# Kernel tuning notes

Hardware: AMD Instinct MI355X
Metric: run time of the kernel (lower is better)

## Reference

```python
import jax, jax.numpy as jnp
import numpy as np

B, L, H, D = 64, 2048, 1024, 128  # segments, segment length, hidden, input_dim
N = B * L

def swish(z):
    return z * jax.nn.sigmoid(z)

def setup_inputs() -> dict:
    key = jax.random.key(0)
    ks = jax.random.split(key, 10)
    s = 0.02
    x_seeds = jax.random.normal(ks[0], (N, D), dtype=jnp.float32)
    x_nodes = jax.random.normal(ks[1], (N, D), dtype=jnp.float32)
    W_seed = jax.random.normal(ks[2], (H, D), dtype=jnp.float32) * s
    W_node = jax.random.normal(ks[3], (H, D), dtype=jnp.float32) * s
    W1 = jax.random.normal(ks[4], (H, H), dtype=jnp.float32) * s
    b1 = jnp.zeros((H,), dtype=jnp.float32)
    W2 = jax.random.normal(ks[5], (H, H), dtype=jnp.float32) * s
    b2 = jnp.zeros((H,), dtype=jnp.float32)
    w_ns = jax.random.normal(ks[6], (1, H), dtype=jnp.float32) * s   # node_score_layer (zero-init in src; random for nontrivial baseline)
    W_stop = jax.random.normal(ks[7], (2, H), dtype=jnp.float32) * s  # stopping_score_layer
    starts = jnp.arange(B, dtype=jnp.int32) * L
    indptr = jnp.stack([starts, starts + L, starts + L], axis=1)  # (start, end, candidate_end)
    return {"x_seeds": x_seeds, "x_nodes": x_nodes, "W_seed": W_seed, "W_node": W_node,
            "W1": W1, "b1": b1, "W2": W2, "b2": b2, "w_ns": w_ns, "W_stop": W_stop,
            "indptr": indptr}

def reference(x_seeds, x_nodes, W_seed, W_node, W1, b1, W2, b2, w_ns, W_stop, indptr):
    # embeddings + 2-layer Swish MLP
    h = x_seeds @ W_seed.T + x_nodes @ W_node.T            # [N, H]
    h = swish(h @ W1.T + b1)
    h = swish(h @ W2.T + b2)
    node_scores = (h @ w_ns.T)[:, 0]                       # [N]
    # ragged segments (uniform length L) defined by indptr starts
    nb = indptr.shape[0]
    seg_len = h.shape[0] // nb                             # static L
    idx = indptr[:, 0][:, None] + jnp.arange(seg_len)      # [B, L]
    h_seg = h[idx]                                         # [B, L, H]
    stop_node = h_seg.mean(axis=1)                         # [B, H] per-segment mean pool
    node_logits = jax.nn.log_softmax(node_scores[idx], axis=1)          # [B, L]
    stop_logits = jax.nn.log_softmax(stop_node @ W_stop.T, axis=1)      # [B, 2]
    # concat([node_logits + stop0, stop1]) per segment
    return jnp.concatenate([node_logits + stop_logits[:, :1], stop_logits[:, 1:]], axis=1)  # [B, L+1]
```

## Files before the change

### kernel.cpp

```cpp
#include <hip/hip_runtime.h>

typedef float f32x4 __attribute__((ext_vector_type(4)));
typedef __bf16 bf16x8 __attribute__((ext_vector_type(8)));
typedef unsigned short u16x8 __attribute__((ext_vector_type(8)));

#define DEVINL static __device__ __forceinline__

DEVINL unsigned short f2bf(float f) {
    unsigned int u = __builtin_bit_cast(unsigned int, f);
    u += 0x7fffu + ((u >> 16) & 1u);
    return (unsigned short)(u >> 16);
}
DEVINL float bf2f(unsigned short u) {
    unsigned int x = ((unsigned int)u) << 16;
    return __builtin_bit_cast(float, x);
}

#define GLD16(gp, lp)                                                          \
    __builtin_amdgcn_global_load_lds(                                          \
        (const __attribute__((address_space(1))) void*)(gp),                   \
        (__attribute__((address_space(3))) void*)(lp), 16, 0, 0)

__global__ void pack_cat_k(const float* __restrict__ s0, const float* __restrict__ s1,
                           unsigned short* __restrict__ dst, int nchunks) {
    int e = blockIdx.x * 256 + threadIdx.x;
    if (e >= nchunks) return;
    int row = e >> 5, ch = e & 31;
    const float* src = (ch < 16) ? (s0 + (size_t)row * 128 + ch * 8)
                                 : (s1 + (size_t)row * 128 + (ch - 16) * 8);
    float4 a = *(const float4*)src;
    float4 b = *(const float4*)(src + 4);
    u16x8 o;
    o[0] = f2bf(a.x); o[1] = f2bf(a.y); o[2] = f2bf(a.z); o[3] = f2bf(a.w);
    o[4] = f2bf(b.x); o[5] = f2bf(b.y); o[6] = f2bf(b.z); o[7] = f2bf(b.w);
    *(u16x8*)(dst + (size_t)e * 8) = o;
}

__global__ void cvt_k(const float* __restrict__ s, unsigned short* __restrict__ d, int nchunks) {
    int e = blockIdx.x * 256 + threadIdx.x;
    if (e >= nchunks) return;
    float4 a = *(const float4*)(s + (size_t)e * 8);
    float4 b = *(const float4*)(s + (size_t)e * 8 + 4);
    u16x8 o;
    o[0] = f2bf(a.x); o[1] = f2bf(a.y); o[2] = f2bf(a.z); o[3] = f2bf(a.w);
    o[4] = f2bf(b.x); o[5] = f2bf(b.y); o[6] = f2bf(b.z); o[7] = f2bf(b.w);
    *(u16x8*)(d + (size_t)e * 8) = o;
}

template <int EPI>
__global__ void gemm_bt_k(const unsigned short* __restrict__ A,
                          const unsigned short* __restrict__ B,
                          const float* __restrict__ bias,
                          unsigned short* __restrict__ C,
                          const float* __restrict__ wns,
                          float* __restrict__ sc,
                          float* __restrict__ pl,
                          int M, int N, int K) {
    __shared__ unsigned short As[128 * 32];
    __shared__ unsigned short Bs[128 * 32];
    const int tid  = threadIdx.x;
    const int lane = tid & 63;
    const int wv   = tid >> 6;
    const int wr   = wv >> 1, wc = wv & 1;
    const int ntn  = N >> 7;

    const int nwg = gridDim.x;
    const int xcd = blockIdx.x & 7, blk = blockIdx.x >> 3;
    const int q = nwg >> 3, rr = nwg & 7;
    const int logical = (xcd < rr ? xcd * (q + 1) : rr * (q + 1) + (xcd - rr) * q) + blk;

    const int im   = logical / ntn, in = logical % ntn;
    const size_t rowA0 = (size_t)im * 128, rowB0 = (size_t)in * 128;

    const int e0 = tid, e1 = tid + 256;
    const int ra0 = e0 >> 2, ca0 = (e0 & 3) * 8;
    const int ra1 = e1 >> 2, ca1 = (e1 & 3) * 8;

    f32x4 acc[4][4] = {};

    const int frow = lane & 15;
    const int kb   = (lane >> 4) * 8;

    for (int k0 = 0; k0 < K; k0 += 32) {
        GLD16(A + (rowA0 + ra0) * K + k0 + ca0, (char*)As + e0 * 16);
        GLD16(A + (rowA0 + ra1) * K + k0 + ca1, (char*)As + e1 * 16);
        GLD16(B + (rowB0 + ra0) * K + k0 + ca0, (char*)Bs + e0 * 16);
        GLD16(B + (rowB0 + ra1) * K + k0 + ca1, (char*)Bs + e1 * 16);
        __syncthreads();

        bf16x8 af[4], bfr[4];
#pragma unroll
        for (int m = 0; m < 4; ++m)
            af[m] = *(const bf16x8*)&As[(wr * 64 + m * 16 + frow) * 32 + kb];
#pragma unroll
        for (int n = 0; n < 4; ++n)
            bfr[n] = *(const bf16x8*)&Bs[(wc * 64 + n * 16 + frow) * 32 + kb];
#pragma unroll
        for (int m = 0; m < 4; ++m)
#pragma unroll
            for (int n = 0; n < 4; ++n)
                acc[m][n] = __builtin_amdgcn_mfma_f32_16x16x32_bf16(af[m], bfr[n], acc[m][n], 0, 0, 0);
        __syncthreads();
    }

    const int r4 = (lane >> 4) * 4;
    const int cc = lane & 15;

    if (EPI == 2) {
#pragma unroll
        for (int n = 0; n < 4; ++n) {
            const float bv = bias[(int)rowB0 + wc * 64 + n * 16 + cc];
#pragma unroll
            for (int m = 0; m < 4; ++m)
#pragma unroll
                for (int r = 0; r < 4; ++r) {
                    float v = acc[m][n][r] + bv;
                    acc[m][n][r] = v / (1.0f + __expf(-v));
                }
        }
#pragma unroll
        for (int m = 0; m < 4; ++m)
#pragma unroll
            for (int r = 0; r < 4; ++r) {
                float s = 0.f;
#pragma unroll
                for (int n = 0; n < 4; ++n)
                    s += acc[m][n][r] * wns[(int)rowB0 + wc * 64 + n * 16 + cc];
#pragma unroll
                for (int o = 1; o < 16; o <<= 1) s += __shfl_xor(s, o);
                if (cc == 0)
                    atomicAdd(&sc[rowA0 + wr * 64 + m * 16 + r4 + r], s);
            }
        const int seg = (int)(rowA0 >> 11);
#pragma unroll
        for (int n = 0; n < 4; ++n) {
            float p = 0.f;
#pragma unroll
            for (int m = 0; m < 4; ++m)
#pragma unroll
                for (int r = 0; r < 4; ++r) p += acc[m][n][r];
            p += __shfl_xor(p, 16);
            p += __shfl_xor(p, 32);
            if ((lane >> 4) == 0)
                atomicAdd(&pl[seg * 1024 + (int)rowB0 + wc * 64 + n * 16 + cc],
                          p * (1.0f / 2048.0f));
        }
        return;
    }

#pragma unroll
    for (int n = 0; n < 4; ++n) {
        const int col = (int)rowB0 + wc * 64 + n * 16 + cc;
        const float bv = (EPI == 1) ? bias[col] : 0.0f;
#pragma unroll
        for (int m = 0; m < 4; ++m) {
            const size_t row = rowA0 + wr * 64 + m * 16 + r4;
#pragma unroll
            for (int r = 0; r < 4; ++r) {
                float v = acc[m][n][r] + bv;
                if (EPI == 1) v = v / (1.0f + __expf(-v));
                C[(row + r) * (size_t)N + col] = f2bf(v);
            }
        }
    }
}

__global__ void stop_k(const float* __restrict__ pool, const float* __restrict__ Wstop,
                       float* __restrict__ stp, float* __restrict__ out) {
    const int b = blockIdx.x, t = threadIdx.x;
    float a0 = 0.f, a1 = 0.f;
#pragma unroll
    for (int j = 0; j < 4; ++j) {
        const int hcol = t + j * 256;
        const float pv = pool[b * 1024 + hcol];
        a0 += pv * Wstop[hcol];
        a1 += pv * Wstop[1024 + hcol];
    }
    const int lane = t & 63, wv = t >> 6;
#pragma unroll
    for (int off = 32; off; off >>= 1) { a0 += __shfl_down(a0, off); a1 += __shfl_down(a1, off); }
    __shared__ float r0[4], r1[4];
    if (lane == 0) { r0[wv] = a0; r1[wv] = a1; }
    __syncthreads();
    if (t == 0) {
        const float s0 = r0[0] + r0[1] + r0[2] + r0[3];
        const float s1 = r1[0] + r1[1] + r1[2] + r1[3];
        const float m  = fmaxf(s0, s1);
        const float lse = m + __logf(__expf(s0 - m) + __expf(s1 - m));
        stp[b * 2] = s0 - lse;
        out[(size_t)b * 2049 + 2048] = s1 - lse;
    }
}

__global__ void node_k(const float* __restrict__ sc, const float* __restrict__ stp,
                       float* __restrict__ out) {
    const int b = blockIdx.x, t = threadIdx.x;
    const float* s = sc + (size_t)b * 2048;
    float v[8];
    float mx = -3.4e38f;
#pragma unroll
    for (int j = 0; j < 8; ++j) { v[j] = s[t + j * 256]; mx = fmaxf(mx, v[j]); }
    const int lane = t & 63, wv = t >> 6;
    __shared__ float red[4];
#pragma unroll
    for (int off = 32; off; off >>= 1) mx = fmaxf(mx, __shfl_down(mx, off));
    if (lane == 0) red[wv] = mx;
    __syncthreads();
    mx = fmaxf(fmaxf(red[0], red[1]), fmaxf(red[2], red[3]));
    float se = 0.f;
#pragma unroll
    for (int j = 0; j < 8; ++j) se += __expf(v[j] - mx);
    __syncthreads();
#pragma unroll
    for (int off = 32; off; off >>= 1) se += __shfl_down(se, off);
    if (lane == 0) red[wv] = se;
    __syncthreads();
    se = red[0] + red[1] + red[2] + red[3];
    const float base = stp[b * 2] - mx - __logf(se);
#pragma unroll
    for (int j = 0; j < 8; ++j) out[(size_t)b * 2049 + t + j * 256] = v[j] + base;
}

extern "C" void kernel_launch(void* const* d_in, const int* in_sizes, int n_in,
                              void* d_out, int out_size, void* d_ws, size_t ws_size,
                              hipStream_t stream) {
    (void)in_sizes; (void)n_in; (void)out_size;
    const float* x_seeds = (const float*)d_in[0];
    const float* x_nodes = (const float*)d_in[1];
    const float* W_seed  = (const float*)d_in[2];
    const float* W_node  = (const float*)d_in[3];
    const float* W1      = (const float*)d_in[4];
    const float* b1      = (const float*)d_in[5];
    const float* W2      = (const float*)d_in[6];
    const float* b2      = (const float*)d_in[7];
    const float* w_ns    = (const float*)d_in[8];
    const float* W_stop  = (const float*)d_in[9];
    float* out = (float*)d_out;

    const int N = 131072, H = 1024, B = 64;

    char* ws = (char*)d_ws;
    size_t off = 0;
    auto alloc = [&](size_t bytes) {
        char* p = ws + off;
        off += (bytes + 255) & ~(size_t)255;
        return p;
    };
    unsigned short* wcat = (unsigned short*)alloc((size_t)H * 256 * 2);
    unsigned short* W1b  = (unsigned short*)alloc((size_t)H * H * 2);
    unsigned short* W2b  = (unsigned short*)alloc((size_t)H * H * 2);
    float* scores = (float*)alloc((size_t)N * 4);
    float* pool   = (float*)alloc((size_t)B * H * 4);
    float* stp    = (float*)alloc((size_t)B * 2 * 4);

    const size_t per_row = 256 * 2 + 1024 * 2 + 1024 * 2;
    size_t avail = (ws_size > off + (1u << 20)) ? (ws_size - off - (1u << 20)) : 0;
    long long mc_ll = (long long)(avail / per_row) / 2048 * 2048;
    int Mc = (int)(mc_ll < 2048 ? 2048 : (mc_ll > 65536 ? 65536 : mc_ll));

    unsigned short* xcat_c = (unsigned short*)alloc((size_t)Mc * 256 * 2);
    unsigned short* h0_c   = (unsigned short*)alloc((size_t)Mc * H * 2);
    unsigned short* h1_c   = (unsigned short*)alloc((size_t)Mc * H * 2);

    hipMemsetAsync(pool, 0, (size_t)B * H * 4, stream);
    hipMemsetAsync(scores, 0, (size_t)N * 4, stream);

    pack_cat_k<<<(H * 32) / 256, 256, 0, stream>>>(W_seed, W_node, wcat, H * 32);
    cvt_k<<<(H * H / 8) / 256, 256, 0, stream>>>(W1, W1b, H * H / 8);
    cvt_k<<<(H * H / 8) / 256, 256, 0, stream>>>(W2, W2b, H * H / 8);

    for (int base = 0; base < N; base += Mc) {
        const int m = (N - base < Mc) ? (N - base) : Mc;
        pack_cat_k<<<(m * 32) / 256, 256, 0, stream>>>(
            x_seeds + (size_t)base * 128, x_nodes + (size_t)base * 128, xcat_c, m * 32);
        const int grid = (m / 128) * (H / 128);
        gemm_bt_k<0><<<grid, 256, 0, stream>>>(xcat_c, wcat, nullptr, h0_c,
                                               nullptr, nullptr, nullptr, m, H, 256);
        gemm_bt_k<1><<<grid, 256, 0, stream>>>(h0_c, W1b, b1, h1_c,
                                               nullptr, nullptr, nullptr, m, H, H);
        gemm_bt_k<2><<<grid, 256, 0, stream>>>(h1_c, W2b, b2, nullptr,
                                               w_ns, scores + base,
                                               pool + (size_t)(base / 2048) * H, m, H, H);
    }

    stop_k<<<B, 256, 0, stream>>>(pool, W_stop, stp, out);
    node_k<<<B, 256, 0, stream>>>(scores, stp, out);
}
```

Measured before the change: 1.013 ms.

## Add 256x256 multi-buffered MFMA GEMM kernel for the two HxH layers

Introduces gemm256_k, a 512-thread, 256x256-tile bf16 GEMM that uses 128KB of dynamic LDS split into K-half buffers. It interleaves global-to-LDS async loads with MFMA phases, using explicit vmcnt waits, barriers and setprio. LDS addresses are XOR-swizzled to avoid bank conflicts. The W1 and W2 layers, including the fused swish, score-dot and pooling epilogues, move to this kernel to raise arithmetic intensity and overlap memory with compute. The trade-offs are heavy register and LDS pressure, with occupancy of at most two blocks per CU, and more complex synchronisation.

```diff
diff --git a/kernel.cpp b/kernel.cpp
--- a/kernel.cpp
+++ b/kernel.cpp
@@ -52,9 +52,6 @@
                           const unsigned short* __restrict__ B,
                           const float* __restrict__ bias,
                           unsigned short* __restrict__ C,
-                          const float* __restrict__ wns,
-                          float* __restrict__ sc,
-                          float* __restrict__ pl,
                           int M, int N, int K) {
     __shared__ unsigned short As[128 * 32];
     __shared__ unsigned short Bs[128 * 32];
@@ -77,7 +74,6 @@
     const int ra1 = e1 >> 2, ca1 = (e1 & 3) * 8;
 
     f32x4 acc[4][4] = {};
-
     const int frow = lane & 15;
     const int kb   = (lane >> 4) * 8;
 
@@ -105,13 +101,133 @@
 
     const int r4 = (lane >> 4) * 4;
     const int cc = lane & 15;
+#pragma unroll
+    for (int n = 0; n < 4; ++n) {
+        const int col = (int)rowB0 + wc * 64 + n * 16 + cc;
+        const float bv = (EPI == 1) ? bias[col] : 0.0f;
+#pragma unroll
+        for (int m = 0; m < 4; ++m) {
+            const size_t row = rowA0 + wr * 64 + m * 16 + r4;
+#pragma unroll
+            for (int r = 0; r < 4; ++r) {
+                float v = acc[m][n][r] + bv;
+                if (EPI == 1) v = v / (1.0f + __expf(-v));
+                C[(row + r) * (size_t)N + col] = f2bf(v);
+            }
+        }
+    }
+}
+
+DEVINL int swz(int b) { return b ^ (((b >> 9) & 1) << 5); }
+
+template <int BS, int KH, int MH>
+DEVINL void phase_mfma(char* smA, char* smB, f32x4 (&acc)[8][4],
+                       int wr, int wc, int fr, int kl) {
+    bf16x8 aF[4], bF[4];
+    char* Ab = smA + BS * 32768 + KH * 16384;
+    char* Bb = smB + BS * 32768 + KH * 16384;
+#pragma unroll
+    for (int x = 0; x < 4; ++x) {
+        const int ba = (wr * 128 + MH * 64 + x * 16 + fr) * 64 + kl;
+        aF[x] = *(const bf16x8*)(Ab + swz(ba));
+        const int bb = (wc * 64 + x * 16 + fr) * 64 + kl;
+        bF[x] = *(const bf16x8*)(Bb + swz(bb));
+    }
+    __builtin_amdgcn_s_barrier();
+    __builtin_amdgcn_s_setprio(1);
+#pragma unroll
+    for (int m2 = 0; m2 < 4; ++m2)
+#pragma unroll
+        for (int n = 0; n < 4; ++n)
+            acc[MH * 4 + m2][n] = __builtin_amdgcn_mfma_f32_16x16x32_bf16(
+                aF[m2], bF[n], acc[MH * 4 + m2][n], 0, 0, 0);
+    __builtin_amdgcn_s_setprio(0);
+    __builtin_amdgcn_s_barrier();
+}
+
+#define VMW asm volatile("s_waitcnt vmcnt(4)" ::: "memory")
+
+template <int EPI>
+__launch_bounds__(512, 2)
+__global__ void gemm256_k(const unsigned short* __restrict__ A,
+                          const unsigned short* __restrict__ Bm,
+                          const float* __restrict__ bias,
+                          unsigned short* __restrict__ C,
+                          const float* __restrict__ wns,
+                          float* __restrict__ sc,
+                          float* __restrict__ pl,
+                          int M, int N, int K) {
+    extern __shared__ __align__(16) char sm[];
+    char* smA = sm;
+    char* smB = sm + 65536;
+    const int tid  = threadIdx.x;
+    const int lane = tid & 63, w = tid >> 6;
+    const int wr = w >> 2, wc = w & 3;
+    const int fr = lane & 15;
+    const int kl = (lane >> 4) * 16;
+    const int ntn = N >> 8;
+
+    const int nwg = gridDim.x;
+    const int xcd = blockIdx.x & 7, blk = blockIdx.x >> 3;
+    const int q = nwg >> 3, rr = nwg & 7;
+    const int logical = (xcd < rr ? xcd * (q + 1) : rr * (q + 1) + (xcd - rr) * q) + blk;
+    const int im = logical / ntn, in = logical % ntn;
+    const size_t rowA0 = (size_t)im * 256, colB0 = (size_t)in * 256;
+    const int NT = K >> 6;
+
+    f32x4 acc[8][4] = {};
+
+    auto stage = [&](const unsigned short* G, size_t grow0, int tile, int half, char* dst) {
+#pragma unroll
+        for (int j = 0; j < 2; ++j) {
+            const int c = tid + j * 512;
+            const int g = c ^ (((c >> 5) & 1) << 1);
+            GLD16(G + (grow0 + (g >> 2)) * K + tile * 64 + half * 32 + (g & 3) * 8,
+                  dst + c * 16);
+        }
+    };
+
+    stage(A, rowA0, 0, 0, smA);
+    stage(Bm, colB0, 0, 0, smB);
+    stage(A, rowA0, 0, 1, smA + 16384);
+    stage(Bm, colB0, 0, 1, smB + 16384);
+    stage(A, rowA0, 1, 0, smA + 32768);
+    stage(Bm, colB0, 1, 0, smB + 32768);
+    VMW;
+    __builtin_amdgcn_s_barrier();
+
+    const int NI = NT >> 1;
+    for (int i = 0; i < NI; ++i) {
+        const int t1 = 2 * i + 1, t2 = 2 * i + 2, t3 = 2 * i + 3;
+        stage(A, rowA0, t1, 1, smA + 49152);
+        phase_mfma<0, 0, 0>(smA, smB, acc, wr, wc, fr, kl);
+        stage(Bm, colB0, t1, 1, smB + 49152);
+        phase_mfma<0, 0, 1>(smA, smB, acc, wr, wc, fr, kl);
+        if (t2 < NT) stage(A, rowA0, t2, 0, smA);
+        phase_mfma<0, 1, 0>(smA, smB, acc, wr, wc, fr, kl);
+        if (t2 < NT) stage(Bm, colB0, t2, 0, smB);
+        VMW;
+        phase_mfma<0, 1, 1>(smA, smB, acc, wr, wc, fr, kl);
+        if (t2 < NT) stage(A, rowA0, t2, 1, smA + 16384);
+        phase_mfma<1, 0, 0>(smA, smB, acc, wr, wc, fr, kl);
+        if (t2 < NT) stage(Bm, colB0, t2, 1, smB + 16384);
+        phase_mfma<1, 0, 1>(smA, smB, acc, wr, wc, fr, kl);
+        if (t3 < NT) stage(A, rowA0, t3, 0, smA + 32768);
+        phase_mfma<1, 1, 0>(smA, smB, acc, wr, wc, fr, kl);
+        if (t3 < NT) stage(Bm, colB0, t3, 0, smB + 32768);
+        VMW;
+        phase_mfma<1, 1, 1>(smA, smB, acc, wr, wc, fr, kl);
+    }
+
+    const int r4 = (lane >> 4) * 4;
+    const int cc = lane & 15;
 
     if (EPI == 2) {
 #pragma unroll
         for (int n = 0; n < 4; ++n) {
-            const float bv = bias[(int)rowB0 + wc * 64 + n * 16 + cc];
-#pragma unroll
-            for (int m = 0; m < 4; ++m)
+            const float bv = bias[(int)colB0 + wc * 64 + n * 16 + cc];
+#pragma unroll
+            for (int m = 0; m < 8; ++m)
 #pragma unroll
                 for (int r = 0; r < 4; ++r) {
                     float v = acc[m][n][r] + bv;
@@ -119,30 +235,30 @@
                 }
         }
 #pragma unroll
-        for (int m = 0; m < 4; ++m)
+        for (int m = 0; m < 8; ++m)
 #pragma unroll
             for (int r = 0; r < 4; ++r) {
                 float s = 0.f;
 #pragma unroll
                 for (int n = 0; n < 4; ++n)
-                    s += acc[m][n][r] * wns[(int)rowB0 + wc * 64 + n * 16 + cc];
+                    s += acc[m][n][r] * wns[(int)colB0 + wc * 64 + n * 16 + cc];
 #pragma unroll
                 for (int o = 1; o < 16; o <<= 1) s += __shfl_xor(s, o);
                 if (cc == 0)
-                    atomicAdd(&sc[rowA0 + wr * 64 + m * 16 + r4 + r], s);
+                    atomicAdd(&sc[rowA0 + wr * 128 + m * 16 + r4 + r], s);
             }
         const int seg = (int)(rowA0 >> 11);
 #pragma unroll
         for (int n = 0; n < 4; ++n) {
             float p = 0.f;
 #pragma unroll
-            for (int m = 0; m < 4; ++m)
+            for (int m = 0; m < 8; ++m)
 #pragma unroll
                 for (int r = 0; r < 4; ++r) p += acc[m][n][r];
             p += __shfl_xor(p, 16);
             p += __shfl_xor(p, 32);
             if ((lane >> 4) == 0)
-                atomicAdd(&pl[seg * 1024 + (int)rowB0 + wc * 64 + n * 16 + cc],
+                atomicAdd(&pl[seg * 1024 + (int)colB0 + wc * 64 + n * 16 + cc],
                           p * (1.0f / 2048.0f));
         }
         return;
@@ -150,15 +266,15 @@
 
 #pragma unroll
     for (int n = 0; n < 4; ++n) {
-        const int col = (int)rowB0 + wc * 64 + n * 16 + cc;
-        const float bv = (EPI == 1) ? bias[col] : 0.0f;
-#pragma unroll
-        for (int m = 0; m < 4; ++m) {
-            const size_t row = rowA0 + wr * 64 + m * 16 + r4;
+        const int col = (int)colB0 + wc * 64 + n * 16 + cc;
+        const float bv = bias[col];
+#pragma unroll
+        for (int m = 0; m < 8; ++m) {
+            const size_t row = rowA0 + wr * 128 + m * 16 + r4;
 #pragma unroll
             for (int r = 0; r < 4; ++r) {
                 float v = acc[m][n][r] + bv;
-                if (EPI == 1) v = v / (1.0f + __expf(-v));
+                v = v / (1.0f + __expf(-v));
                 C[(row + r) * (size_t)N + col] = f2bf(v);
             }
         }
@@ -239,6 +355,12 @@
 
     const int N = 131072, H = 1024, B = 64;
 
+    {
+        auto f1 = gemm256_k<1>; auto f2 = gemm256_k<2>;
+        hipFuncSetAttribute((const void*)f1, hipFuncAttributeMaxDynamicSharedMemorySize, 131072);
+        hipFuncSetAttribute((const void*)f2, hipFuncAttributeMaxDynamicSharedMemorySize, 131072);
+    }
+
     char* ws = (char*)d_ws;
     size_t off = 0;
     auto alloc = [&](size_t bytes) {
@@ -273,14 +395,14 @@
         const int m = (N - base < Mc) ? (N - base) : Mc;
         pack_cat_k<<<(m * 32) / 256, 256, 0, stream>>>(
             x_seeds + (size_t)base * 128, x_nodes + (size_t)base * 128, xcat_c, m * 32);
-        const int grid = (m / 128) * (H / 128);
-        gemm_bt_k<0><<<grid, 256, 0, stream>>>(xcat_c, wcat, nullptr, h0_c,
-                                               nullptr, nullptr, nullptr, m, H, 256);
-        gemm_bt_k<1><<<grid, 256, 0, stream>>>(h0_c, W1b, b1, h1_c,
-                                               nullptr, nullptr, nullptr, m, H, H);
-        gemm_bt_k<2><<<grid, 256, 0, stream>>>(h1_c, W2b, b2, nullptr,
-                                               w_ns, scores + base,
-                                               pool + (size_t)(base / 2048) * H, m, H, H);
+        const int grid128 = (m / 128) * (H / 128);
+        gemm_bt_k<0><<<grid128, 256, 0, stream>>>(xcat_c, wcat, nullptr, h0_c, m, H, 256);
+        const int grid256 = (m / 256) * (H / 256);
+        gemm256_k<1><<<grid256, 512, 131072, stream>>>(h0_c, W1b, b1, h1_c,
+                                                       nullptr, nullptr, nullptr, m, H, H);
+        gemm256_k<2><<<grid256, 512, 131072, stream>>>(h1_c, W2b, b2, nullptr,
+                                                       w_ns, scores + base,
+                                                       pool + (size_t)(base / 2048) * H, m, H, H);
     }
 
     stop_k<<<B, 256, 0, stream>>>(pool, W_stop, stp, out);
```

Result: slower. 1.062 ms (+4.8%).
